# Kernel tuning notes

Hardware: AMD Instinct MI355X
Metric: run time of the kernel (lower is better)

The kernel has to match this reference:

```python
import math
import jax, jax.numpy as jnp
import numpy as np

B, S, H, NH = 2, 2048, 1024, 16
HD = H // NH


def setup_inputs() -> dict:
    key = jax.random.key(0)
    k1, k2, k3 = jax.random.split(key, 3)
    scale = 1.0 / math.sqrt(H)
    return {
        "hidden_states": jax.random.normal(k1, (B, S, H), dtype=jnp.float32),
        "attention_mask": jnp.ones((B, 1, S, S), dtype=jnp.float32),
        "qkv_w": jax.random.normal(k2, (3 * H, H), dtype=jnp.float32) * scale,
        "qkv_b": jnp.zeros((3 * H,), dtype=jnp.float32),
        "dense_w": jax.random.normal(k3, (H, H), dtype=jnp.float32) * scale,
        "dense_b": jnp.zeros((H,), dtype=jnp.float32),
    }


def reference(hidden_states, attention_mask, qkv_w, qkv_b, dense_w, dense_b):
    # qkv projection: torch Linear y = x @ W^T + b
    mixed = hidden_states @ qkv_w.T + qkv_b            # [B,S,3H]
    mixed = mixed.reshape(B, S, NH, 3 * HD).transpose(0, 2, 1, 3)  # [B,NH,S,3HD]
    q, k, v = jnp.split(mixed, 3, axis=-1)             # each [B,NH,S,HD]
    scores = jnp.einsum("bhqd,bhkd->bhqk", q, k) / math.sqrt(HD)
    scores = scores * attention_mask - 10000.0 * (1.0 - attention_mask)
    probs = jax.nn.softmax(scores, axis=-1)            # dropout p=0 -> identity
    ctx = jnp.einsum("bhqk,bhkd->bhqd", probs, v)      # [B,NH,S,HD]
    ctx = ctx.transpose(0, 2, 1, 3).reshape(B, S, H)
    out = ctx @ dense_w.T + dense_b                    # output dropout p=0
    return out
```

## Files before the change

kernel.cpp:

```cpp
#include <hip/hip_runtime.h>
#include <hip/hip_bf16.h>
#include <stdint.h>

#define BB 2
#define SS 2048
#define HH 1024
#define NHH 16
#define HDD 64
#define MM (BB*SS)
#define N1 (3*HH)
#define NT (SS/64)
#define LOG2E 1.44269504f

using bf16 = __hip_bfloat16;
typedef __attribute__((ext_vector_type(8))) short bf16x8;
typedef __attribute__((ext_vector_type(4))) float f32x4;

__device__ inline unsigned short f2bfu(float f) {
  union { bf16 h; unsigned short u; } c;
  c.h = __float2bfloat16(f);
  return c.u;
}

__device__ inline unsigned int cvtpk(float lo, float hi) {
  unsigned int r;
  asm("v_cvt_pk_bf16_f32 %0, %1, %2" : "=v"(r) : "v"(lo), "v"(hi));
  return r;
}

__device__ inline void load_lds16(const void* g, void* l) {
  __builtin_amdgcn_global_load_lds(
      (const __attribute__((address_space(1))) void*)g,
      (__attribute__((address_space(3))) void*)l, 16, 0, 0);
}

__device__ inline f32x4 mfma16(bf16x8 a, bf16x8 b, f32x4 c) {
  return __builtin_amdgcn_mfma_f32_16x16x32_bf16(a, b, c, 0, 0, 0);
}

__global__ __launch_bounds__(256) void cvt_f32_bf16(const float* __restrict__ in,
                                                    unsigned short* __restrict__ out,
                                                    int n4) {
  int i = blockIdx.x * blockDim.x + threadIdx.x;
  int st = gridDim.x * blockDim.x;
  for (; i < n4; i += st) {
    float4 v = reinterpret_cast<const float4*>(in)[i];
    ushort4 o;
    o.x = f2bfu(v.x); o.y = f2bfu(v.y); o.z = f2bfu(v.z); o.w = f2bfu(v.w);
    reinterpret_cast<ushort4*>(out)[i] = o;
  }
}

__global__ __launch_bounds__(256) void mask_flags_kernel(const float* __restrict__ mask,
                                                         unsigned char* __restrict__ flags) {
  int t = blockIdx.x;
  int b = t >> 10, qt = (t >> 5) & 31, kt = t & 31;
  const float* mb = mask + ((size_t)b * SS + qt * 64) * SS + kt * 64;
  int row = threadIdx.x >> 2, c0 = (threadIdx.x & 3) * 16;
  int ok = 1;
#pragma unroll
  for (int j = 0; j < 4; ++j) {
    float4 v = *reinterpret_cast<const float4*>(mb + (size_t)row * SS + c0 + j * 4);
    ok &= (v.x == 1.f) & (v.y == 1.f) & (v.z == 1.f) & (v.w == 1.f);
  }
  ok = __all(ok);
  __shared__ int s[4];
  if ((threadIdx.x & 63) == 0) s[threadIdx.x >> 6] = ok;
  __syncthreads();
  if (threadIdx.x == 0) flags[t] = (unsigned char)(s[0] & s[1] & s[2] & s[3]);
}

template <bool OUT_BF16, bool QKV_SPLIT>
__global__ __launch_bounds__(256) void gemm_bt(const unsigned short* __restrict__ A,
                                               const unsigned short* __restrict__ Bt,
                                               const float* __restrict__ bias,
                                               void* __restrict__ Cv,
                                               unsigned short* __restrict__ vT,
                                               int Ndim, int Kdim) {
  __shared__ __align__(16) unsigned short As[128 * 32];
  __shared__ __align__(16) unsigned short Bs[128 * 32];

  const int tid = threadIdx.x;
  const int wave = tid >> 6, lane = tid & 63;
  const int m0 = blockIdx.x * 128;
  const int n0 = blockIdx.y * 128;
  const int wm = (wave >> 1) * 64, wn = (wave & 1) * 64;
  const int lrow = lane & 15;
  const int lk8 = (lane >> 4) * 8;
  const int r4 = (lane >> 4) * 4;

  f32x4 acc[4][4];
  const f32x4 z = {0.f, 0.f, 0.f, 0.f};
  for (int i = 0; i < 4; ++i)
    for (int j = 0; j < 4; ++j) acc[i][j] = z;

  for (int k0 = 0; k0 < Kdim; k0 += 32) {
#pragma unroll
    for (int it = 0; it < 2; ++it) {
      int idx = it * 256 + tid;
      int row = idx >> 2, seg = idx & 3;
      load_lds16(A + (size_t)(m0 + row) * Kdim + k0 + seg * 8, &As[row * 32 + seg * 8]);
      load_lds16(Bt + (size_t)(n0 + row) * Kdim + k0 + seg * 8, &Bs[row * 32 + seg * 8]);
    }
    __syncthreads();

    bf16x8 af[4], bfr[4];
#pragma unroll
    for (int i = 0; i < 4; ++i)
      af[i] = *reinterpret_cast<const bf16x8*>(&As[(wm + i * 16 + lrow) * 32 + lk8]);
#pragma unroll
    for (int j = 0; j < 4; ++j)
      bfr[j] = *reinterpret_cast<const bf16x8*>(&Bs[(wn + j * 16 + lrow) * 32 + lk8]);
#pragma unroll
    for (int i = 0; i < 4; ++i)
#pragma unroll
      for (int j = 0; j < 4; ++j)
        acc[i][j] = mfma16(af[i], bfr[j], acc[i][j]);
    __syncthreads();
  }

#pragma unroll
  for (int i = 0; i < 4; ++i) {
#pragma unroll
    for (int j = 0; j < 4; ++j) {
      int col = n0 + wn + j * 16 + lrow;
      float bv = bias[col];
      int hcol = 0, rr = 0;
      if (QKV_SPLIT) { hcol = col / 192; rr = col - hcol * 192; }
#pragma unroll
      for (int r = 0; r < 4; ++r) {
        int row = m0 + wm + i * 16 + r4 + r;
        float v = acc[i][j][r] + bv;
        if (QKV_SPLIT && rr >= 128) {
          int bb = row >> 11, s = row & (SS - 1);
          vT[(((size_t)bb * NHH + hcol) * HDD + (rr - 128)) * SS + s] = f2bfu(v);
        } else if (OUT_BF16) {
          ((unsigned short*)Cv)[(size_t)row * Ndim + col] = f2bfu(v);
        } else {
          ((float*)Cv)[(size_t)row * Ndim + col] = v;
        }
      }
    }
  }
}

__global__ __launch_bounds__(256, 4) void attn_kernel(const unsigned short* __restrict__ mixed,
                                                      const unsigned short* __restrict__ vT,
                                                      const float* __restrict__ mask,
                                                      const unsigned char* __restrict__ flags,
                                                      unsigned short* __restrict__ ctx) {
  __shared__ __align__(16) unsigned short Ks[2][64 * 64];
  __shared__ __align__(16) unsigned short Vt[2][64 * 64];
  __shared__ __align__(16) unsigned short QP[64 * 64];

  const int tid = threadIdx.x, wave = tid >> 6, lane = tid & 63;
  const int ql = lane & 15;
  const int g = lane >> 4;
  const int q0 = blockIdx.x * 64;
  const int bh = blockIdx.y;
  const int b = bh / NHH, hh = bh % NHH;

  const unsigned short* qbase = mixed + (size_t)(b * SS) * N1 + hh * 192;
  const unsigned short* kbase = qbase + 64;
  const unsigned short* vtbase = vT + ((size_t)(b * NHH + hh) * HDD) * SS;
  const float* mbase = mask + (size_t)b * SS * SS;
  const unsigned char* fl = flags + ((size_t)b * 32 + blockIdx.x) * 32;

  const int srow = tid >> 3, sseg = tid & 7;
  const int swst = (sseg ^ (srow & 7)) << 3;

  load_lds16(qbase + (size_t)(q0 + srow) * N1 + swst, &QP[srow * 64 + sseg * 8]);
  load_lds16(qbase + (size_t)(q0 + 32 + srow) * N1 + swst, &QP[(32 + srow) * 64 + sseg * 8]);
  load_lds16(kbase + (size_t)srow * N1 + swst, &Ks[0][srow * 64 + sseg * 8]);
  load_lds16(kbase + (size_t)(32 + srow) * N1 + swst, &Ks[0][(32 + srow) * 64 + sseg * 8]);
  load_lds16(vtbase + (size_t)srow * SS + swst, &Vt[0][srow * 64 + sseg * 8]);
  load_lds16(vtbase + (size_t)(32 + srow) * SS + swst, &Vt[0][(32 + srow) * 64 + sseg * 8]);
  __syncthreads();

  const int qrow = wave * 16 + ql;
  const bf16x8 qf0 = *reinterpret_cast<const bf16x8*>(
      &QP[qrow * 64 + ((g ^ (qrow & 7)) << 3)]);
  const bf16x8 qf1 = *reinterpret_cast<const bf16x8*>(
      &QP[qrow * 64 + (((g + 4) ^ (qrow & 7)) << 3)]);
  __syncthreads();

  const int s0 = (g ^ (ql & 7)) << 3;
  const int s1 = ((g + 4) ^ (ql & 7)) << 3;
  const unsigned short* KrA = &Ks[0][ql * 64 + s0];
  const unsigned short* KrB = &Ks[0][ql * 64 + s1];
  const unsigned short* VrA = &Vt[0][ql * 64 + s0];
  const unsigned short* VrB = &Vt[0][ql * 64 + s1];
  unsigned short* Ps = &QP[wave * 1024];
  const int X = (ql & 7) << 3;
  unsigned short* Pw0 = &Ps[ql * 64 + ((4 * g) ^ X)];
  unsigned short* Pw1 = &Ps[ql * 64 + ((16 + 4 * g) ^ X)];
  unsigned short* Pw2 = &Ps[ql * 64 + ((32 + 4 * g) ^ X)];
  unsigned short* Pw3 = &Ps[ql * 64 + ((48 + 4 * g) ^ X)];
  const unsigned short* Pr0 = &Ps[ql * 64 + ((8 * g) ^ X)];
  const unsigned short* Pr1 = &Ps[ql * 64 + ((32 + 8 * g) ^ X)];

  const unsigned short* kpre = kbase + (size_t)(64 + srow) * N1 + swst;
  const unsigned short* vpre = vtbase + (size_t)srow * SS + 64 + swst;

  f32x4 oacc[4];
  const f32x4 z = {0.f, 0.f, 0.f, 0.f};
  for (int fd = 0; fd < 4; ++fd) oacc[fd] = z;
  float lsum = 0.f;
  const float C2 = 0.125f * LOG2E;

#define TILE_BODY(CUR_, KT_, HAVENEXT_)                                         \
  {                                                                             \
    const int kt_ = (KT_);                                                      \
    if (HAVENEXT_) {                                                            \
      load_lds16(kpre, &Ks[(CUR_)^1][srow * 64 + sseg * 8]);                    \
      load_lds16(kpre + 32 * N1, &Ks[(CUR_)^1][(32 + srow) * 64 + sseg * 8]);   \
      load_lds16(vpre, &Vt[(CUR_)^1][srow * 64 + sseg * 8]);                    \
      load_lds16(vpre + 32 * SS, &Vt[(CUR_)^1][(32 + srow) * 64 + sseg * 8]);   \
    }                                                                           \
    kpre += 64 * N1; vpre += 64;                                                \
    f32x4 sacc[4];                                                              \
    __builtin_amdgcn_s_setprio(1);                                              \
    _Pragma("unroll")                                                           \
    for (int n = 0; n < 4; ++n) {                                               \
      bf16x8 k0 = *reinterpret_cast<const bf16x8*>(KrA + (CUR_)*4096 + n*1024); \
      bf16x8 k1 = *reinterpret_cast<const bf16x8*>(KrB + (CUR_)*4096 + n*1024); \
      sacc[n] = mfma16(k0, qf0, z);                                             \
      sacc[n] = mfma16(k1, qf1, sacc[n]);                                       \
    }                                                                           \
    __builtin_amdgcn_s_setprio(0);                                              \
    const bool allones = fl[kt_] != 0;                                          \
    float pv[4][4];                                                             \
    if (allones) {                                                              \
      _Pragma("unroll")                                                         \
      for (int n = 0; n < 4; ++n)                                               \
        _Pragma("unroll")                                                       \
        for (int r = 0; r < 4; ++r)                                             \
          pv[n][r] = exp2f(sacc[n][r] * C2);                                    \
    } else {                                                                    \
      int qq = q0 + wave * 16 + ql;                                             \
      _Pragma("unroll")                                                         \
      for (int n = 0; n < 4; ++n)                                               \
        _Pragma("unroll")                                                       \
        for (int r = 0; r < 4; ++r) {                                           \
          int kk = kt_ * 64 + 16 * n + 4 * g + r;                               \
          float mv = mbase[(size_t)qq * SS + kk];                               \
          float s = sacc[n][r] * 0.125f;                                        \
          pv[n][r] = exp2f((s * mv - 10000.f * (1.f - mv)) * LOG2E);            \
        }                                                                       \
    }                                                                           \
                                 \
    {                                                                           \
      float t00 = (pv[0][0] + pv[0][1]) + (pv[0][2] + pv[0][3]);                \
      float t01 = (pv[1][0] + pv[1][1]) + (pv[1][2] + pv[1][3]);                \
      float t10 = (pv[2][0] + pv[2][1]) + (pv[2][2] + pv[2][3]);                \
      float t11 = (pv[3][0] + pv[3][1]) + (pv[3][2] + pv[3][3]);                \
      lsum += (t00 + t01) + (t10 + t11);                                        \
    }                                                                           \
    { uint2 w; w.x = cvtpk(pv[0][0], pv[0][1]); w.y = cvtpk(pv[0][2], pv[0][3]);\
      *reinterpret_cast<uint2*>(Pw0) = w; }                                     \
    { uint2 w; w.x = cvtpk(pv[1][0], pv[1][1]); w.y = cvtpk(pv[1][2], pv[1][3]);\
      *reinterpret_cast<uint2*>(Pw1) = w; }                                     \
    { uint2 w; w.x = cvtpk(pv[2][0], pv[2][1]); w.y = cvtpk(pv[2][2], pv[2][3]);\
      *reinterpret_cast<uint2*>(Pw2) = w; }                                     \
    { uint2 w; w.x = cvtpk(pv[3][0], pv[3][1]); w.y = cvtpk(pv[3][2], pv[3][3]);\
      *reinterpret_cast<uint2*>(Pw3) = w; }                                     \
    bf16x8 pa0 = *reinterpret_cast<const bf16x8*>(Pr0);                         \
    bf16x8 pa1 = *reinterpret_cast<const bf16x8*>(Pr1);                         \
    __builtin_amdgcn_s_setprio(1);                                              \
    _Pragma("unroll")                                                           \
    for (int fd = 0; fd < 4; ++fd) {                                            \
      bf16x8 bv0 = *reinterpret_cast<const bf16x8*>(VrA + (CUR_)*4096 + fd*1024);\
      bf16x8 bv1 = *reinterpret_cast<const bf16x8*>(VrB + (CUR_)*4096 + fd*1024);\
      oacc[fd] = mfma16(pa0, bv0, oacc[fd]);                                    \
      oacc[fd] = mfma16(pa1, bv1, oacc[fd]);                                    \
    }                                                                           \
    __builtin_amdgcn_s_setprio(0);                                              \
    __syncthreads();                                                            \
  }

  for (int kt = 0; kt < NT; kt += 2) {
    TILE_BODY(0, kt, true)
    TILE_BODY(1, kt + 1, (kt + 2 < NT))
  }
#undef TILE_BODY

  float lrun = lsum;
  lrun += __shfl_xor(lrun, 16, 64);
  lrun += __shfl_xor(lrun, 32, 64);
  float invl = 1.f / lrun;
#pragma unroll
  for (int r = 0; r < 4; ++r) {
    float inv = __shfl(invl, g * 4 + r, 64);
    int qq = q0 + wave * 16 + g * 4 + r;
    unsigned short* cp = ctx + (size_t)(b * SS + qq) * HH + hh * HDD;
#pragma unroll
    for (int fd = 0; fd < 4; ++fd)
      cp[fd * 16 + ql] = f2bfu(oacc[fd][r] * inv);
  }
}

extern "C" void kernel_launch(void* const* d_in, const int* in_sizes, int n_in,
                              void* d_out, int out_size, void* d_ws, size_t ws_size,
                              hipStream_t stream) {
  const float* hs      = (const float*)d_in[0];
  const float* mask    = (const float*)d_in[1];
  const float* qkv_w   = (const float*)d_in[2];
  const float* qkv_b   = (const float*)d_in[3];
  const float* dense_w = (const float*)d_in[4];
  const float* dense_b = (const float*)d_in[5];
  float* out = (float*)d_out;

  char* ws = (char*)d_ws;
  unsigned short* hs_b     = (unsigned short*)(ws);
  unsigned short* qkvw_b   = (unsigned short*)(ws + 8388608);
  unsigned short* densew_b = (unsigned short*)(ws + 14680064);
  unsigned short* mixed_b  = (unsigned short*)(ws + 16777216);
  unsigned short* ctx_b    = (unsigned short*)(ws + 41943040);
  unsigned char*  flags    = (unsigned char*)(ws + 50331648);
  unsigned short* vT_b     = (unsigned short*)(ws + 50335744);

  cvt_f32_bf16<<<2048, 256, 0, stream>>>(hs, hs_b, (MM * HH) / 4);
  cvt_f32_bf16<<<2048, 256, 0, stream>>>(qkv_w, qkvw_b, (N1 * HH) / 4);
  cvt_f32_bf16<<<1024, 256, 0, stream>>>(dense_w, densew_b, (HH * HH) / 4);
  mask_flags_kernel<<<BB * 32 * 32, 256, 0, stream>>>(mask, flags);

  gemm_bt<true, true><<<dim3(MM / 128, N1 / 128), 256, 0, stream>>>(
      hs_b, qkvw_b, qkv_b, mixed_b, vT_b, N1, HH);

  attn_kernel<<<dim3(SS / 64, BB * NHH), 256, 0, stream>>>(
      mixed_b, vT_b, mask, flags, ctx_b);

  gemm_bt<false, false><<<dim3(MM / 128, HH / 128), 256, 0, stream>>>(
      ctx_b, densew_b, dense_b, out, nullptr, HH, HH);
}
```

Measured before the change: 158.4 us.

## Process 128 query rows per attention block to reuse K/V tiles

Each attention block now handles two 64-row query groups (128 rows), and each wave computes two independent 16-row strips against the same K and V fragments loaded from LDS. This halves the number of blocks and the global/LDS traffic for K and V per query row. In exchange it doubles accumulator and register pressure, lowers launch bounds occupancy to 2, and enlarges the Q/P shared buffer. The grid shrinks to 512 blocks, which may underfill the GPU.

Result: no change. 161.1 us (+1.7%).

```diff
diff --git a/kernel.cpp b/kernel.cpp
--- a/kernel.cpp
+++ b/kernel.cpp
@@ -144,19 +144,19 @@
   }
 }
 
-__global__ __launch_bounds__(256, 4) void attn_kernel(const unsigned short* __restrict__ mixed,
+__global__ __launch_bounds__(256, 2) void attn_kernel(const unsigned short* __restrict__ mixed,
                                                       const unsigned short* __restrict__ vT,
                                                       const float* __restrict__ mask,
                                                       const unsigned char* __restrict__ flags,
                                                       unsigned short* __restrict__ ctx) {
   __shared__ __align__(16) unsigned short Ks[2][64 * 64];
   __shared__ __align__(16) unsigned short Vt[2][64 * 64];
-  __shared__ __align__(16) unsigned short QP[64 * 64];
+  __shared__ __align__(16) unsigned short QP[128 * 64];
 
   const int tid = threadIdx.x, wave = tid >> 6, lane = tid & 63;
   const int ql = lane & 15;
   const int g = lane >> 4;
-  const int q0 = blockIdx.x * 64;
+  const int q0 = blockIdx.x * 128;
   const int bh = blockIdx.y;
   const int b = bh / NHH, hh = bh % NHH;
 
@@ -164,13 +164,19 @@
   const unsigned short* kbase = qbase + 64;
   const unsigned short* vtbase = vT + ((size_t)(b * NHH + hh) * HDD) * SS;
   const float* mbase = mask + (size_t)b * SS * SS;
-  const unsigned char* fl = flags + ((size_t)b * 32 + blockIdx.x) * 32;
+  const unsigned char* fl0 = flags + ((size_t)b * 32 + blockIdx.x * 2) * 32;
+  const unsigned char* fl1 = fl0 + 32;
 
   const int srow = tid >> 3, sseg = tid & 7;
   const int swst = (sseg ^ (srow & 7)) << 3;
 
-  load_lds16(qbase + (size_t)(q0 + srow) * N1 + swst, &QP[srow * 64 + sseg * 8]);
-  load_lds16(qbase + (size_t)(q0 + 32 + srow) * N1 + swst, &QP[(32 + srow) * 64 + sseg * 8]);
+#pragma unroll
+  for (int it = 0; it < 4; ++it) {
+    int idx = it * 256 + tid;
+    int row = idx >> 3, seg = idx & 7;
+    load_lds16(qbase + (size_t)(q0 + row) * N1 + ((seg ^ (row & 7)) << 3),
+               &QP[row * 64 + seg * 8]);
+  }
   load_lds16(kbase + (size_t)srow * N1 + swst, &Ks[0][srow * 64 + sseg * 8]);
   load_lds16(kbase + (size_t)(32 + srow) * N1 + swst, &Ks[0][(32 + srow) * 64 + sseg * 8]);
   load_lds16(vtbase + (size_t)srow * SS + swst, &Vt[0][srow * 64 + sseg * 8]);
@@ -178,10 +184,14 @@
   __syncthreads();
 
   const int qrow = wave * 16 + ql;
-  const bf16x8 qf0 = *reinterpret_cast<const bf16x8*>(
+  const bf16x8 qfA0 = *reinterpret_cast<const bf16x8*>(
       &QP[qrow * 64 + ((g ^ (qrow & 7)) << 3)]);
-  const bf16x8 qf1 = *reinterpret_cast<const bf16x8*>(
+  const bf16x8 qfA1 = *reinterpret_cast<const bf16x8*>(
       &QP[qrow * 64 + (((g + 4) ^ (qrow & 7)) << 3)]);
+  const bf16x8 qfB0 = *reinterpret_cast<const bf16x8*>(
+      &QP[(64 + qrow) * 64 + ((g ^ (qrow & 7)) << 3)]);
+  const bf16x8 qfB1 = *reinterpret_cast<const bf16x8*>(
+      &QP[(64 + qrow) * 64 + (((g + 4) ^ (qrow & 7)) << 3)]);
   __syncthreads();
 
   const int s0 = (g ^ (ql & 7)) << 3;
@@ -190,22 +200,29 @@
   const unsigned short* KrB = &Ks[0][ql * 64 + s1];
   const unsigned short* VrA = &Vt[0][ql * 64 + s0];
   const unsigned short* VrB = &Vt[0][ql * 64 + s1];
-  unsigned short* Ps = &QP[wave * 1024];
+  unsigned short* PsA = &QP[wave * 1024];
+  unsigned short* PsB = &QP[4096 + wave * 1024];
   const int X = (ql & 7) << 3;
-  unsigned short* Pw0 = &Ps[ql * 64 + ((4 * g) ^ X)];
-  unsigned short* Pw1 = &Ps[ql * 64 + ((16 + 4 * g) ^ X)];
-  unsigned short* Pw2 = &Ps[ql * 64 + ((32 + 4 * g) ^ X)];
-  unsigned short* Pw3 = &Ps[ql * 64 + ((48 + 4 * g) ^ X)];
-  const unsigned short* Pr0 = &Ps[ql * 64 + ((8 * g) ^ X)];
-  const unsigned short* Pr1 = &Ps[ql * 64 + ((32 + 8 * g) ^ X)];
+  unsigned short* PwA0 = &PsA[ql * 64 + ((4 * g) ^ X)];
+  unsigned short* PwA1 = &PsA[ql * 64 + ((16 + 4 * g) ^ X)];
+  unsigned short* PwA2 = &PsA[ql * 64 + ((32 + 4 * g) ^ X)];
+  unsigned short* PwA3 = &PsA[ql * 64 + ((48 + 4 * g) ^ X)];
+  const unsigned short* PrA0 = &PsA[ql * 64 + ((8 * g) ^ X)];
+  const unsigned short* PrA1 = &PsA[ql * 64 + ((32 + 8 * g) ^ X)];
+  unsigned short* PwB0 = PwA0 + 4096;
+  unsigned short* PwB1 = PwA1 + 4096;
+  unsigned short* PwB2 = PwA2 + 4096;
+  unsigned short* PwB3 = PwA3 + 4096;
+  const unsigned short* PrB0 = PrA0 + 4096;
+  const unsigned short* PrB1 = PrA1 + 4096;
 
   const unsigned short* kpre = kbase + (size_t)(64 + srow) * N1 + swst;
   const unsigned short* vpre = vtbase + (size_t)srow * SS + 64 + swst;
 
-  f32x4 oacc[4];
+  f32x4 oaccA[4], oaccB[4];
   const f32x4 z = {0.f, 0.f, 0.f, 0.f};
-  for (int fd = 0; fd < 4; ++fd) oacc[fd] = z;
-  float lsum = 0.f;
+  for (int fd = 0; fd < 4; ++fd) { oaccA[fd] = z; oaccB[fd] = z; }
+  float lsumA = 0.f, lsumB = 0.f;
   const float C2 = 0.125f * LOG2E;
 
 #define TILE_BODY(CUR_, KT_, HAVENEXT_)                                         \
@@ -218,61 +235,84 @@
       load_lds16(vpre + 32 * SS, &Vt[(CUR_)^1][(32 + srow) * 64 + sseg * 8]);   \
     }                                                                           \
     kpre += 64 * N1; vpre += 64;                                                \
-    f32x4 sacc[4];                                                              \
+    f32x4 saccA[4], saccB[4];                                                   \
     __builtin_amdgcn_s_setprio(1);                                              \
     _Pragma("unroll")                                                           \
     for (int n = 0; n < 4; ++n) {                                               \
       bf16x8 k0 = *reinterpret_cast<const bf16x8*>(KrA + (CUR_)*4096 + n*1024); \
       bf16x8 k1 = *reinterpret_cast<const bf16x8*>(KrB + (CUR_)*4096 + n*1024); \
-      sacc[n] = mfma16(k0, qf0, z);                                             \
-      sacc[n] = mfma16(k1, qf1, sacc[n]);                                       \
+      saccA[n] = mfma16(k0, qfA0, z);                                           \
+      saccA[n] = mfma16(k1, qfA1, saccA[n]);                                    \
+      saccB[n] = mfma16(k0, qfB0, z);                                           \
+      saccB[n] = mfma16(k1, qfB1, saccB[n]);                                    \
     }                                                                           \
     __builtin_amdgcn_s_setprio(0);                                              \
-    const bool allones = fl[kt_] != 0;                                          \
-    float pv[4][4];                                                             \
+    const bool allones = (fl0[kt_] & fl1[kt_]) != 0;                            \
+    float pvA[4][4], pvB[4][4];                                                 \
     if (allones) {                                                              \
       _Pragma("unroll")                                                         \
       for (int n = 0; n < 4; ++n)                                               \
         _Pragma("unroll")                                                       \
-        for (int r = 0; r < 4; ++r)                                             \
-          pv[n][r] = exp2f(sacc[n][r] * C2);                                    \
+        for (int r = 0; r < 4; ++r) {                                           \
+          pvA[n][r] = exp2f(saccA[n][r] * C2);                                  \
+          pvB[n][r] = exp2f(saccB[n][r] * C2);                                  \
+        }                                                                       \
     } else {                                                                    \
-      int qq = q0 + wave * 16 + ql;                                             \
+      int qqA = q0 + wave * 16 + ql;                                            \
       _Pragma("unroll")                                                         \
       for (int n = 0; n < 4; ++n)                                               \
         _Pragma("unroll")                                                       \
         for (int r = 0; r < 4; ++r) {                                           \
           int kk = kt_ * 64 + 16 * n + 4 * g + r;                               \
-          float mv = mbase[(size_t)qq * SS + kk];                               \
-          float s = sacc[n][r] * 0.125f;                                        \
-          pv[n][r] = exp2f((s * mv - 10000.f * (1.f - mv)) * LOG2E);            \
+          float mvA = mbase[(size_t)qqA * SS + kk];                             \
+          float mvB = mbase[(size_t)(qqA + 64) * SS + kk];                      \
+          float sA = saccA[n][r] * 0.125f;                                      \
+          float sB = saccB[n][r] * 0.125f;                                      \
+          pvA[n][r] = exp2f((sA * mvA - 10000.f * (1.f - mvA)) * LOG2E);        \
+          pvB[n][r] = exp2f((sB * mvB - 10000.f * (1.f - mvB)) * LOG2E);        \
         }                                                                       \
     }                                                                           \
-                                 \
     {                                                                           \
-      float t00 = (pv[0][0] + pv[0][1]) + (pv[0][2] + pv[0][3]);                \
-      float t01 = (pv[1][0] + pv[1][1]) + (pv[1][2] + pv[1][3]);                \
-      float t10 = (pv[2][0] + pv[2][1]) + (pv[2][2] + pv[2][3]);                \
-      float t11 = (pv[3][0] + pv[3][1]) + (pv[3][2] + pv[3][3]);                \
-      lsum += (t00 + t01) + (t10 + t11);                                        \
-    }                                                                           \
-    { uint2 w; w.x = cvtpk(pv[0][0], pv[0][1]); w.y = cvtpk(pv[0][2], pv[0][3]);\
-      *reinterpret_cast<uint2*>(Pw0) = w; }                                     \
-    { uint2 w; w.x = cvtpk(pv[1][0], pv[1][1]); w.y = cvtpk(pv[1][2], pv[1][3]);\
-      *reinterpret_cast<uint2*>(Pw1) = w; }                                     \
-    { uint2 w; w.x = cvtpk(pv[2][0], pv[2][1]); w.y = cvtpk(pv[2][2], pv[2][3]);\
-      *reinterpret_cast<uint2*>(Pw2) = w; }                                     \
-    { uint2 w; w.x = cvtpk(pv[3][0], pv[3][1]); w.y = cvtpk(pv[3][2], pv[3][3]);\
-      *reinterpret_cast<uint2*>(Pw3) = w; }                                     \
-    bf16x8 pa0 = *reinterpret_cast<const bf16x8*>(Pr0);                         \
-    bf16x8 pa1 = *reinterpret_cast<const bf16x8*>(Pr1);                         \
+      float tA0 = (pvA[0][0] + pvA[0][1]) + (pvA[0][2] + pvA[0][3]);            \
+      float tA1 = (pvA[1][0] + pvA[1][1]) + (pvA[1][2] + pvA[1][3]);            \
+      float tA2 = (pvA[2][0] + pvA[2][1]) + (pvA[2][2] + pvA[2][3]);            \
+      float tA3 = (pvA[3][0] + pvA[3][1]) + (pvA[3][2] + pvA[3][3]);            \
+      lsumA += (tA0 + tA1) + (tA2 + tA3);                                       \
+      float tB0 = (pvB[0][0] + pvB[0][1]) + (pvB[0][2] + pvB[0][3]);            \
+      float tB1 = (pvB[1][0] + pvB[1][1]) + (pvB[1][2] + pvB[1][3]);            \
+      float tB2 = (pvB[2][0] + pvB[2][1]) + (pvB[2][2] + pvB[2][3]);            \
+      float tB3 = (pvB[3][0] + pvB[3][1]) + (pvB[3][2] + pvB[3][3]);            \
+      lsumB += (tB0 + tB1) + (tB2 + tB3);                                       \
+    }                                                                           \
+    { uint2 w; w.x = cvtpk(pvA[0][0], pvA[0][1]); w.y = cvtpk(pvA[0][2], pvA[0][3]); \
+      *reinterpret_cast<uint2*>(PwA0) = w; }                                    \
+    { uint2 w; w.x = cvtpk(pvA[1][0], pvA[1][1]); w.y = cvtpk(pvA[1][2], pvA[1][3]); \
+      *reinterpret_cast<uint2*>(PwA1) = w; }                                    \
+    { uint2 w; w.x = cvtpk(pvA[2][0], pvA[2][1]); w.y = cvtpk(pvA[2][2], pvA[2][3]); \
+      *reinterpret_cast<uint2*>(PwA2) = w; }                                    \
+    { uint2 w; w.x = cvtpk(pvA[3][0], pvA[3][1]); w.y = cvtpk(pvA[3][2], pvA[3][3]); \
+      *reinterpret_cast<uint2*>(PwA3) = w; }                                    \
+    { uint2 w; w.x = cvtpk(pvB[0][0], pvB[0][1]); w.y = cvtpk(pvB[0][2], pvB[0][3]); \
+      *reinterpret_cast<uint2*>(PwB0) = w; }                                    \
+    { uint2 w; w.x = cvtpk(pvB[1][0], pvB[1][1]); w.y = cvtpk(pvB[1][2], pvB[1][3]); \
+      *reinterpret_cast<uint2*>(PwB1) = w; }                                    \
+    { uint2 w; w.x = cvtpk(pvB[2][0], pvB[2][1]); w.y = cvtpk(pvB[2][2], pvB[2][3]); \
+      *reinterpret_cast<uint2*>(PwB2) = w; }                                    \
+    { uint2 w; w.x = cvtpk(pvB[3][0], pvB[3][1]); w.y = cvtpk(pvB[3][2], pvB[3][3]); \
+      *reinterpret_cast<uint2*>(PwB3) = w; }                                    \
+    bf16x8 paA0 = *reinterpret_cast<const bf16x8*>(PrA0);                       \
+    bf16x8 paA1 = *reinterpret_cast<const bf16x8*>(PrA1);                       \
+    bf16x8 paB0 = *reinterpret_cast<const bf16x8*>(PrB0);                       \
+    bf16x8 paB1 = *reinterpret_cast<const bf16x8*>(PrB1);                       \
     __builtin_amdgcn_s_setprio(1);                                              \
     _Pragma("unroll")                                                           \
     for (int fd = 0; fd < 4; ++fd) {                                            \
-      bf16x8 bv0 = *reinterpret_cast<const bf16x8*>(VrA + (CUR_)*4096 + fd*1024);\
-      bf16x8 bv1 = *reinterpret_cast<const bf16x8*>(VrB + (CUR_)*4096 + fd*1024);\
-      oacc[fd] = mfma16(pa0, bv0, oacc[fd]);                                    \
-      oacc[fd] = mfma16(pa1, bv1, oacc[fd]);                                    \
+      bf16x8 bv0 = *reinterpret_cast<const bf16x8*>(VrA + (CUR_)*4096 + fd*1024); \
+      bf16x8 bv1 = *reinterpret_cast<const bf16x8*>(VrB + (CUR_)*4096 + fd*1024); \
+      oaccA[fd] = mfma16(paA0, bv0, oaccA[fd]);                                 \
+      oaccA[fd] = mfma16(paA1, bv1, oaccA[fd]);                                 \
+      oaccB[fd] = mfma16(paB0, bv0, oaccB[fd]);                                 \
+      oaccB[fd] = mfma16(paB1, bv1, oaccB[fd]);                                 \
     }                                                                           \
     __builtin_amdgcn_s_setprio(0);                                              \
     __syncthreads();                                                            \
@@ -284,18 +324,22 @@
   }
 #undef TILE_BODY
 
-  float lrun = lsum;
-  lrun += __shfl_xor(lrun, 16, 64);
-  lrun += __shfl_xor(lrun, 32, 64);
-  float invl = 1.f / lrun;
+  float lA = lsumA, lB = lsumB;
+  lA += __shfl_xor(lA, 16, 64); lA += __shfl_xor(lA, 32, 64);
+  lB += __shfl_xor(lB, 16, 64); lB += __shfl_xor(lB, 32, 64);
+  float invA = 1.f / lA, invB = 1.f / lB;
 #pragma unroll
   for (int r = 0; r < 4; ++r) {
-    float inv = __shfl(invl, g * 4 + r, 64);
-    int qq = q0 + wave * 16 + g * 4 + r;
-    unsigned short* cp = ctx + (size_t)(b * SS + qq) * HH + hh * HDD;
-#pragma unroll
-    for (int fd = 0; fd < 4; ++fd)
-      cp[fd * 16 + ql] = f2bfu(oacc[fd][r] * inv);
+    float iA = __shfl(invA, g * 4 + r, 64);
+    float iB = __shfl(invB, g * 4 + r, 64);
+    int qqA = q0 + wave * 16 + g * 4 + r;
+    unsigned short* cpA = ctx + (size_t)(b * SS + qqA) * HH + hh * HDD;
+    unsigned short* cpB = ctx + (size_t)(b * SS + qqA + 64) * HH + hh * HDD;
+#pragma unroll
+    for (int fd = 0; fd < 4; ++fd) {
+      cpA[fd * 16 + ql] = f2bfu(oaccA[fd][r] * iA);
+      cpB[fd * 16 + ql] = f2bfu(oaccB[fd][r] * iB);
+    }
   }
 }
 
@@ -327,7 +371,7 @@
   gemm_bt<true, true><<<dim3(MM / 128, N1 / 128), 256, 0, stream>>>(
       hs_b, qkvw_b, qkv_b, mixed_b, vT_b, N1, HH);
 
-  attn_kernel<<<dim3(SS / 64, BB * NHH), 256, 0, stream>>>(
+  attn_kernel<<<dim3(SS / 128, BB * NHH), 256, 0, stream>>>(
       mixed_b, vT_b, mask, flags, ctx_b);
 
   gemm_bt<false, false><<<dim3(MM / 128, HH / 128), 256, 0, stream>>>(
```
